# Optimization experiments

Hardware: AMD Instinct MI355X
Metric: run time of the kernel (lower is better)

The kernel has to match this reference:

```python
import jax, jax.numpy as jnp
import numpy as np

N, C, H, W = 8, 80, 200, 200
PRE_NMS_THRESH = 0.05
PRE_NMS_TOP_N = 1000
NMS_THRESH = 0.6
FPN_POST_NMS_TOP_N = 100
MIN_SIZE = 0.0
TO_REMOVE = 1.0
CLASS_OFFSET = 100000.0  # > any coordinate; separates classes for class-aware NMS


def setup_inputs() -> dict:
    key = jax.random.key(0)
    k1, k2, k3, k4, k5 = jax.random.split(key, 5)
    # logits shifted so sigmoid probs sit near the 0.05 threshold (realistic sparsity)
    box_cls = jax.random.normal(k1, (N, C, H, W), jnp.float32) - 3.0
    box_regression = jax.random.uniform(k2, (N, 4, H, W), jnp.float32) * 64.0
    centerness = jax.random.normal(k3, (N, 1, H, W), jnp.float32)
    locations = jax.random.uniform(k4, (H * W, 2), jnp.float32) * 1600.0
    image_sizes = jax.random.randint(k5, (N, 2), 800, 1600, jnp.int32)  # (h, w)
    return {"locations": locations, "box_cls": box_cls,
            "box_regression": box_regression, "centerness": centerness,
            "image_sizes": image_sizes}


def _pairwise_iou(boxes):
    x1, y1, x2, y2 = boxes[:, 0], boxes[:, 1], boxes[:, 2], boxes[:, 3]
    area = (x2 - x1 + TO_REMOVE) * (y2 - y1 + TO_REMOVE)  # [K]
    iw = jnp.clip(jnp.minimum(x2[:, None], x2[None, :]) - jnp.maximum(x1[:, None], x1[None, :]) + TO_REMOVE, 0.0)
    ih = jnp.clip(jnp.minimum(y2[:, None], y2[None, :]) - jnp.maximum(y1[:, None], y1[None, :]) + TO_REMOVE, 0.0)
    inter = iw * ih
    return inter / (area[:, None] + area[None, :] - inter)


def reference(locations, box_cls, box_regression, centerness, image_sizes):
    n, c, h, w = box_cls.shape
    # [N,C,H,W] -> [N,HW,C] probs; [N,4,H,W] -> [N,HW,4]; centerness -> [N,HW]
    cls_prob = jax.nn.sigmoid(box_cls.transpose(0, 2, 3, 1).reshape(n, -1, c))
    reg = box_regression.transpose(0, 2, 3, 1).reshape(n, -1, 4)
    cent = jax.nn.sigmoid(centerness.transpose(0, 2, 3, 1).reshape(n, -1))

    def per_image(p, r, ct, hw):
        # candidate mask on raw class probs (before centerness weighting), as in source
        cand = p > PRE_NMS_THRESH                      # [HW, C]
        scores = p * ct[:, None]                       # [HW, C]
        flat = jnp.where(cand, scores, -jnp.inf).reshape(-1)
        top_s, top_i = jax.lax.top_k(flat, PRE_NMS_TOP_N)   # sorted desc
        loc_idx = top_i // c
        labels = top_i % c + 1
        valid = top_s > 0.0
        l2 = locations[loc_idx]                        # [K, 2]
        rr = r[loc_idx]                                # [K, 4]
        boxes = jnp.concatenate([l2 - rr[:, :2], l2 + rr[:, 2:]], axis=-1)
        ih = hw[0].astype(jnp.float32)
        iw = hw[1].astype(jnp.float32)
        boxes = jnp.stack([jnp.clip(boxes[:, 0], 0.0, iw - 1.0),
                           jnp.clip(boxes[:, 1], 0.0, ih - 1.0),
                           jnp.clip(boxes[:, 2], 0.0, iw - 1.0),
                           jnp.clip(boxes[:, 3], 0.0, ih - 1.0)], axis=-1)
        bw = boxes[:, 2] - boxes[:, 0] + TO_REMOVE
        bh = boxes[:, 3] - boxes[:, 1] + TO_REMOVE
        valid = valid & (bw >= MIN_SIZE) & (bh >= MIN_SIZE)
        # class-aware NMS via per-class coordinate offset
        ob = boxes + labels.astype(jnp.float32)[:, None] * CLASS_OFFSET
        iou = _pairwise_iou(ob)                        # [K, K]
        K = PRE_NMS_TOP_N
        idxs = jnp.arange(K)
        def body(supp, i):
            keep_i = valid[i] & jnp.logical_not(supp[i])
            supp = supp | (keep_i & (iou[i] > NMS_THRESH) & (idxs != i))
            return supp, keep_i
        _, keep = jax.lax.scan(body, jnp.zeros(K, dtype=bool), idxs)
        fscores = jnp.where(keep & valid, top_s, -jnp.inf)
        fs, fi = jax.lax.top_k(fscores, FPN_POST_NMS_TOP_N)
        fv = fs > 0.0
        fb = boxes[fi] * fv[:, None].astype(boxes.dtype)
        fl = jnp.where(fv, labels[fi], 0).astype(jnp.float32)
        out_s = jnp.where(fv, jnp.sqrt(jnp.where(fv, fs, 1.0)), 0.0)  # sqrt of cls*centerness
        # [K_post, 6] = x1,y1,x2,y2,score,label
        return jnp.concatenate([fb, out_s[:, None], fl[:, None]], axis=-1)

    return jax.vmap(per_image)(cls_prob, reg, cent, image_sizes)
```

## Files before the change

### kernel.cpp

```cpp
#include <hip/hip_runtime.h>
#include <math.h>

#define NIMG 8
#define NCLS 80
#define HW 40000
#define M (NCLS*HW)
#define UBINS 4096
#define CANDL 4096
#define SPILL_CAP 65536
#define BCAP 1024
#define TOPK 1000
#define OUTK 100
#define PRE_T 0.05f
#define NMS_T 0.6f
#define FLOOR_S 0.25f
#define FLOOR_BITS 0x3E800000u
#define FLOOR_SAFE 0.2494f

__device__ unsigned int       g_scnt[NIMG][32];
__device__ unsigned int       g_ovf[NIMG];
__device__ float              g_xthr[NIMG * HW];
__device__ float              g_sct[NIMG * HW];
__device__ unsigned long long g_key[NIMG][SPILL_CAP];

__device__ __forceinline__ float sigmoid_exact(float x){
    return 1.0f / (1.0f + expf(-x));
}

__global__ void k0_init(const float* __restrict__ cent){
    int t = blockIdx.x * blockDim.x + threadIdx.x;
    if (t < NIMG * 32) ((unsigned int*)g_scnt)[t] = 0u;
    if (t < NIMG) g_ovf[t] = 0u;
    if (t < NIMG * HW){
        float pct = sigmoid_exact(cent[t]);
        g_sct[t] = pct;
        float a = FLOOR_SAFE / pct;
        float xt;
        if (a >= 1.0f) xt = 3.0e38f;
        else {
            float am = fminf(a, 0.98f);
            xt = logf(am / (1.0f - am));
        }
        g_xthr[t] = xt;
    }
}

__global__ void __launch_bounds__(1024) k1_spill(const float* __restrict__ cls){
    const int n   = blockIdx.y;
    const int tid = threadIdx.x;
    const int e0  = blockIdx.x * 4096 + tid * 4;
    __shared__ unsigned long long skey[BCAP];
    __shared__ unsigned int lcnt, lbase;
    if (tid == 0) lcnt = 0u;
    __syncthreads();
    if (e0 < M){
        const int c  = e0 / HW;
        const int hw = e0 - c * HW;
        float4 x  = *(const float4*)(cls + (size_t)n * M + e0);
        float4 th = *(const float4*)(g_xthr + n * HW + hw);
        #define SPILL1(J, XV) \
        if (XV >= (J==0?th.x:J==1?th.y:J==2?th.z:th.w)){ \
            float p_ = sigmoid_exact(XV); \
            if (p_ > PRE_T){ \
                float s_ = p_ * g_sct[n * HW + hw + J]; \
                unsigned long long key_ = ((unsigned long long)__float_as_uint(s_) << 32) \
                    | (unsigned long long)(0xFFFFFFFFu - (unsigned int)((hw + J) * NCLS + c)); \
                unsigned int pp_ = atomicAdd(&lcnt, 1u); \
                if (pp_ < BCAP) skey[pp_] = key_; \
            } \
        }
        SPILL1(0, x.x)
        SPILL1(1, x.y)
        SPILL1(2, x.z)
        SPILL1(3, x.w)
        #undef SPILL1
    }
    __syncthreads();
    unsigned int raw = lcnt;
    unsigned int cnt = raw < BCAP ? raw : BCAP;
    if (tid == 0){
        lbase = cnt ? atomicAdd(&g_scnt[n][0], cnt) : 0u;
        if (raw > BCAP) g_ovf[n] = 1u;
    }
    __syncthreads();
    unsigned int base = lbase;
    for (unsigned int i = tid; i < cnt; i += 1024){
        unsigned int pos = base + i;
        if (pos < SPILL_CAP) g_key[n][pos] = skey[i];
    }
}

struct SelPhase {
    unsigned int hist[UBINS];
    unsigned int cs[256];
    unsigned long long keysL[CANDL];
};
struct NmsPhase {
    float ox1[TOPK], oy1[TOPK], ox2[TOPK], oy2[TOPK], oar[TOPK];
    float bxs[TOPK][4];
    float sc[TOPK];
    int   lab[TOPK];
    unsigned char validf[TOPK];
    unsigned char supp[TOPK];
    int   keeplist[OUTK];
};
union KU { SelPhase sel; NmsPhase nms; };

__global__ void __launch_bounds__(1024) k2_select_nms(const float* __restrict__ cls,
                                                      const float* __restrict__ loc,
                                                      const float* __restrict__ reg,
                                                      const int*   __restrict__ imsz,
                                                      float* __restrict__ out){
    const int n = blockIdx.x;
    const int tid = threadIdx.x;
    const int lane = tid & 63;
    __shared__ KU u;
    __shared__ unsigned long long stop[TOPK];
    __shared__ unsigned int lcnt, c025, s_cut, s_flag;

    for (int i = tid; i < UBINS; i += 1024) u.sel.hist[i] = 0u;
    if (tid == 0){ lcnt = 0u; c025 = 0u; }
    if (tid < TOPK) stop[tid] = 0ull;
    __syncthreads();

    unsigned int scnt_raw = g_scnt[n][0];
    unsigned int S = scnt_raw < SPILL_CAP ? scnt_raw : SPILL_CAP;

    for (unsigned int i = tid; i < S; i += 1024){
        unsigned long long k = g_key[n][i];
        unsigned int bits = (unsigned int)(k >> 32);
        float s = __uint_as_float(bits);
        int bin = (int)(s * 4096.0f);
        atomicAdd(&u.sel.hist[bin], 1u);
        unsigned long long mb = __ballot(bits >= FLOOR_BITS);
        if (lane == 0 && mb) atomicAdd(&c025, (unsigned int)__popcll(mb));
    }
    __syncthreads();
    if (tid < 256){
        unsigned int s = 0;
        int base = tid * 16;
        #pragma unroll
        for (int i = 0; i < 16; ++i) s += u.sel.hist[base + i];
        u.sel.cs[tid] = s;
    }
    __syncthreads();
    if (tid == 0){
        unsigned int acc = 0; int cut = 0;
        int c = 255;
        for (; c >= 0; --c){ if (acc + u.sel.cs[c] >= TOPK) break; acc += u.sel.cs[c]; }
        unsigned int Cest = 0;
        if (c >= 0){
            int b = c*16 + 15;
            for (;; --b){
                if (acc + u.sel.hist[b] >= TOPK || b == c*16){ cut = b; break; }
                acc += u.sel.hist[b];
            }
            Cest = acc + u.sel.hist[cut];
        }
        unsigned int fl = (scnt_raw > SPILL_CAP) || g_ovf[n] || (c < 0) ||
                          (c025 < TOPK) || (Cest > CANDL) ? 1u : 0u;
        s_cut = (unsigned int)cut; s_flag = fl;
    }
    __syncthreads();

    if (s_flag){
        for (int i = tid; i < UBINS; i += 1024) u.sel.hist[i] = 0u;
        __syncthreads();
        const float* cls_n = cls + (size_t)n * M;
        const float* sct_n = g_sct + n * HW;
        for (int e = tid; e < M; e += 1024){
            float p = sigmoid_exact(cls_n[e]);
            if (p > PRE_T){
                int c = e / HW; int hw = e - c * HW;
                float s = p * sct_n[hw];
                atomicAdd(&u.sel.hist[(int)(s * 4096.0f)], 1u);
            }
        }
        __syncthreads();
        if (tid < 256){
            unsigned int s = 0;
            int base = tid * 16;
            #pragma unroll
            for (int i = 0; i < 16; ++i) s += u.sel.hist[base + i];
            u.sel.cs[tid] = s;
        }
        __syncthreads();
        if (tid == 0){
            unsigned int acc = 0; int cut = 0; int c = 255;
            for (; c >= 0; --c){ if (acc + u.sel.cs[c] >= TOPK) break; acc += u.sel.cs[c]; }
            if (c >= 0){
                int b = c*16 + 15;
                for (;; --b){ acc += u.sel.hist[b]; if (acc >= TOPK || b == c*16) break; }
                cut = b;
            }
            while (acc > CANDL && cut < UBINS){ acc -= u.sel.hist[cut]; cut++; }
            s_cut = (unsigned int)cut;
        }
        __syncthreads();
        unsigned int cutb = s_cut;
        for (int e = tid; e < M; e += 1024){
            float p = sigmoid_exact(cls_n[e]);
            if (p > PRE_T){
                int c = e / HW; int hw = e - c * HW;
                float s = p * sct_n[hw];
                if ((int)(s * 4096.0f) >= (int)cutb){
                    unsigned int pos = atomicAdd(&lcnt, 1u);
                    if (pos < CANDL){
                        unsigned int idx = (unsigned int)(hw * NCLS + c);
                        u.sel.keysL[pos] = ((unsigned long long)__float_as_uint(s) << 32)
                                         | (unsigned long long)(0xFFFFFFFFu - idx);
                    }
                }
            }
        }
    } else {
        unsigned int cutb = s_cut;
        for (unsigned int i = tid; i < S; i += 1024){
            unsigned long long k = g_key[n][i];
            float s = __uint_as_float((unsigned int)(k >> 32));
            bool pass = ((unsigned int)(int)(s * 4096.0f)) >= cutb;
            unsigned long long mb = __ballot(pass);
            unsigned int wcnt = (unsigned int)__popcll(mb);
            unsigned int base = 0;
            if (lane == 0 && wcnt) base = atomicAdd(&lcnt, wcnt);
            base = (unsigned int)__builtin_amdgcn_readfirstlane((int)base);
            if (pass){
                unsigned int p = base + (unsigned int)__popcll(mb & ((1ull << lane) - 1ull));
                if (p < CANDL) u.sel.keysL[p] = k;
            }
        }
    }
    __syncthreads();

    int C = (int)(lcnt < CANDL ? lcnt : CANDL);
    for (int i = tid; i < C; i += 1024){
        unsigned long long k = u.sel.keysL[i];
        int rank = 0;
        for (int j = 0; j < C; ++j) rank += (u.sel.keysL[j] > k) ? 1 : 0;
        if (rank < TOPK) stop[rank] = k;
    }
    __syncthreads();

    float rx1 = 0.f, ry1 = 0.f, rx2 = -1.f, ry2 = -1.f, rar = 1.f;
    float ihh = (float)imsz[2*n + 0];
    float iww = (float)imsz[2*n + 1];
    unsigned long long kk = (tid < TOPK) ? stop[tid] : 0ull;
    __syncthreads();
    if (tid < TOPK){
        unsigned int bits = (unsigned int)(kk >> 32);
        float s = __uint_as_float(bits);
        u.nms.supp[tid] = 0;
        if (s > 0.0f){
            unsigned int idx = 0xFFFFFFFFu - (unsigned int)(kk & 0xFFFFFFFFull);
            int hw = (int)(idx / NCLS);
            int c  = (int)(idx % NCLS);
            int l  = c + 1;
            float x  = loc[2*hw], y = loc[2*hw + 1];
            float r0 = reg[((size_t)n*4 + 0)*HW + hw];
            float r1 = reg[((size_t)n*4 + 1)*HW + hw];
            float r2 = reg[((size_t)n*4 + 2)*HW + hw];
            float r3 = reg[((size_t)n*4 + 3)*HW + hw];
            float x1 = fminf(fmaxf(x - r0, 0.0f), iww - 1.0f);
            float y1 = fminf(fmaxf(y - r1, 0.0f), ihh - 1.0f);
            float x2 = fminf(fmaxf(x + r2, 0.0f), iww - 1.0f);
            float y2 = fminf(fmaxf(y + r3, 0.0f), ihh - 1.0f);
            u.nms.bxs[tid][0] = x1; u.nms.bxs[tid][1] = y1;
            u.nms.bxs[tid][2] = x2; u.nms.bxs[tid][3] = y2;
            float off = (float)l * 100000.0f;
            float a1 = x1 + off, b1 = y1 + off, a2 = x2 + off, b2 = y2 + off;
            float ar = (a2 - a1 + 1.0f) * (b2 - b1 + 1.0f);
            u.nms.ox1[tid] = a1; u.nms.oy1[tid] = b1;
            u.nms.ox2[tid] = a2; u.nms.oy2[tid] = b2; u.nms.oar[tid] = ar;
            rx1 = a1; ry1 = b1; rx2 = a2; ry2 = b2; rar = ar;
            u.nms.sc[tid] = s; u.nms.lab[tid] = l; u.nms.validf[tid] = 1;
        } else {
            u.nms.validf[tid] = 0; u.nms.sc[tid] = 0.0f; u.nms.lab[tid] = 0;
            u.nms.bxs[tid][0] = u.nms.bxs[tid][1] = 0.0f;
            u.nms.bxs[tid][2] = u.nms.bxs[tid][3] = 0.0f;
            u.nms.ox1[tid] = 0.f; u.nms.oy1[tid] = 0.f;
            u.nms.ox2[tid] = -1.f; u.nms.oy2[tid] = -1.f; u.nms.oar[tid] = 1.f;
        }
    }
    __syncthreads();

    int cnt = 0;
    for (int i = 0; i < TOPK; ++i){
        bool keep_i = u.nms.validf[i] && !u.nms.supp[i];
        if (keep_i){
            if (tid == 0) u.nms.keeplist[cnt] = i;
            if (tid < TOPK && tid != i){
                float ix1 = fmaxf(u.nms.ox1[i], rx1);
                float iy1 = fmaxf(u.nms.oy1[i], ry1);
                float ix2 = fminf(u.nms.ox2[i], rx2);
                float iy2 = fminf(u.nms.oy2[i], ry2);
                float iw_ = fmaxf(ix2 - ix1 + 1.0f, 0.0f);
                float ih_ = fmaxf(iy2 - iy1 + 1.0f, 0.0f);
                float inter = iw_ * ih_;
                float iou = inter / (u.nms.oar[i] + rar - inter);
                if (iou > NMS_T) u.nms.supp[tid] = 1;
            }
            cnt++;
            __syncthreads();
            if (cnt == OUTK) break;
        }
    }
    __syncthreads();

    if (tid < OUTK){
        float r0=0.f,r1=0.f,r2=0.f,r3=0.f,r4=0.f,r5=0.f;
        if (tid < cnt){
            int i = u.nms.keeplist[tid];
            r0 = u.nms.bxs[i][0]; r1 = u.nms.bxs[i][1];
            r2 = u.nms.bxs[i][2]; r3 = u.nms.bxs[i][3];
            r4 = sqrtf(u.nms.sc[i]); r5 = (float)u.nms.lab[i];
        }
        float* o = out + ((size_t)n*OUTK + tid)*6;
        o[0]=r0; o[1]=r1; o[2]=r2; o[3]=r3; o[4]=r4; o[5]=r5;
    }
}

extern "C" void kernel_launch(void* const* d_in, const int* in_sizes, int n_in,
                              void* d_out, int out_size, void* d_ws, size_t ws_size,
                              hipStream_t stream){
    const float* loc  = (const float*)d_in[0];
    const float* cls  = (const float*)d_in[1];
    const float* reg  = (const float*)d_in[2];
    const float* cent = (const float*)d_in[3];
    const int*   imsz = (const int*)d_in[4];
    float* out = (float*)d_out;

    hipLaunchKernelGGL(k0_init,       dim3(625),                 dim3(512),  0, stream, cent);
    hipLaunchKernelGGL(k1_spill,      dim3((M+4095)/4096, NIMG), dim3(1024), 0, stream, cls);
    hipLaunchKernelGGL(k2_select_nms, dim3(NIMG),                dim3(1024), 0, stream,
                       cls, loc, reg, imsz, out);
}
```

Measured before the change: 291.5 us.

## Replace rank sort with bitonic sort and parallelize NMS per class in waves

```diff
diff --git a/kernel.cpp b/kernel.cpp
--- a/kernel.cpp
+++ b/kernel.cpp
@@ -100,9 +100,14 @@
     float bxs[TOPK][4];
     float sc[TOPK];
     int   lab[TOPK];
+    int   keeplist[OUTK];
+    unsigned int  Wc[16][80];
+    unsigned int  coff[81];
+    unsigned int  wcnt[16];
+    unsigned short ord[1024];
     unsigned char validf[TOPK];
     unsigned char supp[TOPK];
-    int   keeplist[OUTK];
+    unsigned char keepf[1024];
 };
 union KU { SelPhase sel; NmsPhase nms; };
 
@@ -114,12 +119,13 @@
     const int n = blockIdx.x;
     const int tid = threadIdx.x;
     const int lane = tid & 63;
+    const int wv   = tid >> 6;
     __shared__ KU u;
     __shared__ unsigned long long stop[TOPK];
-    __shared__ unsigned int lcnt, c025, s_cut, s_flag;
+    __shared__ unsigned int lcnt, c025, s_cut, s_flag, s_nmsfb, s_cnt;
 
     for (int i = tid; i < UBINS; i += 1024) u.sel.hist[i] = 0u;
-    if (tid == 0){ lcnt = 0u; c025 = 0u; }
+    if (tid == 0){ lcnt = 0u; c025 = 0u; s_nmsfb = 0u; }
     if (tid < TOPK) stop[tid] = 0ull;
     __syncthreads();
 
@@ -220,9 +226,9 @@
             float s = __uint_as_float((unsigned int)(k >> 32));
             bool pass = ((unsigned int)(int)(s * 4096.0f)) >= cutb;
             unsigned long long mb = __ballot(pass);
-            unsigned int wcnt = (unsigned int)__popcll(mb);
+            unsigned int wcnt_ = (unsigned int)__popcll(mb);
             unsigned int base = 0;
-            if (lane == 0 && wcnt) base = atomicAdd(&lcnt, wcnt);
+            if (lane == 0 && wcnt_) base = atomicAdd(&lcnt, wcnt_);
             base = (unsigned int)__builtin_amdgcn_readfirstlane((int)base);
             if (pass){
                 unsigned int p = base + (unsigned int)__popcll(mb & ((1ull << lane) - 1ull));
@@ -233,11 +239,31 @@
     __syncthreads();
 
     int C = (int)(lcnt < CANDL ? lcnt : CANDL);
-    for (int i = tid; i < C; i += 1024){
-        unsigned long long k = u.sel.keysL[i];
-        int rank = 0;
-        for (int j = 0; j < C; ++j) rank += (u.sel.keysL[j] > k) ? 1 : 0;
-        if (rank < TOPK) stop[rank] = k;
+    if (C <= 2048){
+        int Nsort = (C <= 1024) ? 1024 : 2048;
+        for (int i = C + tid; i < Nsort; i += 1024) u.sel.keysL[i] = 0ull;
+        __syncthreads();
+        for (int k = 2; k <= Nsort; k <<= 1){
+            for (int j = k >> 1; j > 0; j >>= 1){
+                if (tid < (Nsort >> 1)){
+                    int i  = ((tid & ~(j - 1)) << 1) | (tid & (j - 1));
+                    int p2 = i | j;
+                    unsigned long long a = u.sel.keysL[i];
+                    unsigned long long b = u.sel.keysL[p2];
+                    bool up = ((i & k) == 0);
+                    if (up ? (a < b) : (a > b)){ u.sel.keysL[i] = b; u.sel.keysL[p2] = a; }
+                }
+                __syncthreads();
+            }
+        }
+        if (tid < TOPK) stop[tid] = u.sel.keysL[tid];
+    } else {
+        for (int i = tid; i < C; i += 1024){
+            unsigned long long k = u.sel.keysL[i];
+            int rank = 0;
+            for (int j = 0; j < C; ++j) rank += (u.sel.keysL[j] > k) ? 1 : 0;
+            if (rank < TOPK) stop[rank] = k;
+        }
     }
     __syncthreads();
 
@@ -246,6 +272,11 @@
     float iww = (float)imsz[2*n + 1];
     unsigned long long kk = (tid < TOPK) ? stop[tid] : 0ull;
     __syncthreads();
+
+    u.nms.keepf[tid] = 0;
+    { unsigned int* wz = &u.nms.Wc[0][0];
+      for (int i = tid; i < 16*80; i += 1024) wz[i] = 0u; }
+
     if (tid < TOPK){
         unsigned int bits = (unsigned int)(kk >> 32);
         float s = __uint_as_float(bits);
@@ -283,29 +314,115 @@
     }
     __syncthreads();
 
-    int cnt = 0;
-    for (int i = 0; i < TOPK; ++i){
-        bool keep_i = u.nms.validf[i] && !u.nms.supp[i];
-        if (keep_i){
-            if (tid == 0) u.nms.keeplist[cnt] = i;
-            if (tid < TOPK && tid != i){
-                float ix1 = fmaxf(u.nms.ox1[i], rx1);
-                float iy1 = fmaxf(u.nms.oy1[i], ry1);
-                float ix2 = fminf(u.nms.ox2[i], rx2);
-                float iy2 = fminf(u.nms.oy2[i], ry2);
-                float iw_ = fmaxf(ix2 - ix1 + 1.0f, 0.0f);
-                float ih_ = fmaxf(iy2 - iy1 + 1.0f, 0.0f);
-                float inter = iw_ * ih_;
-                float iou = inter / (u.nms.oar[i] + rar - inter);
-                if (iou > NMS_T) u.nms.supp[tid] = 1;
-            }
-            cnt++;
-            __syncthreads();
-            if (cnt == OUTK) break;
-        }
-    }
-    __syncthreads();
-
+    int mk = -1;
+    if (tid < TOPK && u.nms.validf[tid]) mk = u.nms.lab[tid] - 1;
+    if (mk >= 0) atomicAdd(&u.nms.Wc[wv][mk], 1u);
+    __syncthreads();
+    if (tid < NCLS){
+        unsigned int acc = 0;
+        for (int w = 0; w < 16; ++w){
+            unsigned int v = u.nms.Wc[w][tid];
+            u.nms.Wc[w][tid] = acc;
+            acc += v;
+        }
+        u.nms.coff[tid] = acc;
+        if (acc > 64) atomicOr(&s_nmsfb, 1u);
+    }
+    __syncthreads();
+    if (tid == 0){
+        unsigned int acc = 0;
+        for (int k = 0; k < NCLS; ++k){ unsigned int t = u.nms.coff[k]; u.nms.coff[k] = acc; acc += t; }
+        u.nms.coff[NCLS] = acc;
+    }
+    __syncthreads();
+
+    if (!s_nmsfb){
+        int below = 0;
+        for (int l = 0; l < 64; ++l){
+            int ok = __shfl(mk, l);
+            below += (l < lane && ok == mk) ? 1 : 0;
+        }
+        if (mk >= 0){
+            unsigned int pos = u.nms.coff[mk] + u.nms.Wc[wv][mk] + (unsigned int)below;
+            u.nms.ord[pos] = (unsigned short)tid;
+        }
+        __syncthreads();
+
+        for (int k = wv; k < NCLS; k += 16){
+            int base = (int)u.nms.coff[k];
+            int ck   = (int)u.nms.coff[k + 1] - base;
+            if (ck <= 0) continue;
+            int rr = (lane < ck) ? (int)u.nms.ord[base + lane] : -1;
+            float bx1 = 0.f, by1 = 0.f, bx2 = -1.f, by2 = -1.f, bar = 1.f;
+            if (rr >= 0){
+                bx1 = u.nms.ox1[rr]; by1 = u.nms.oy1[rr];
+                bx2 = u.nms.ox2[rr]; by2 = u.nms.oy2[rr]; bar = u.nms.oar[rr];
+            }
+            int sup = 0;
+            for (int p = 0; p < ck; ++p){
+                int keep_p = !__shfl(sup, p);
+                if (keep_p){
+                    float px1 = __shfl(bx1, p), py1 = __shfl(by1, p);
+                    float px2 = __shfl(bx2, p), py2 = __shfl(by2, p);
+                    float par = __shfl(bar, p);
+                    if (lane > p && rr >= 0){
+                        float ix1 = fmaxf(px1, bx1);
+                        float iy1 = fmaxf(py1, by1);
+                        float ix2 = fminf(px2, bx2);
+                        float iy2 = fminf(py2, by2);
+                        float iw_ = fmaxf(ix2 - ix1 + 1.0f, 0.0f);
+                        float ih_ = fmaxf(iy2 - iy1 + 1.0f, 0.0f);
+                        float inter = iw_ * ih_;
+                        float iou = inter / (par + bar - inter);
+                        if (iou > NMS_T) sup = 1;
+                    }
+                }
+            }
+            if (rr >= 0) u.nms.keepf[rr] = sup ? 0 : 1;
+        }
+        __syncthreads();
+
+        int kf = (int)u.nms.keepf[tid];
+        unsigned long long mb = __ballot(kf != 0);
+        if (lane == 0) u.nms.wcnt[wv] = (unsigned int)__popcll(mb);
+        __syncthreads();
+        if (tid == 0){
+            unsigned int acc = 0;
+            for (int w = 0; w < 16; ++w){ unsigned int t = u.nms.wcnt[w]; u.nms.wcnt[w] = acc; acc += t; }
+            s_cnt = acc < OUTK ? acc : OUTK;
+        }
+        __syncthreads();
+        if (kf){
+            unsigned int slot = u.nms.wcnt[wv] + (unsigned int)__popcll(mb & ((1ull << lane) - 1ull));
+            if (slot < OUTK) u.nms.keeplist[slot] = tid;
+        }
+    } else {
+        int cnt = 0;
+        for (int i = 0; i < TOPK; ++i){
+            bool keep_i = u.nms.validf[i] && !u.nms.supp[i];
+            if (keep_i){
+                if (tid == 0) u.nms.keeplist[cnt] = i;
+                if (tid < TOPK && tid != i){
+                    float ix1 = fmaxf(u.nms.ox1[i], rx1);
+                    float iy1 = fmaxf(u.nms.oy1[i], ry1);
+                    float ix2 = fminf(u.nms.ox2[i], rx2);
+                    float iy2 = fminf(u.nms.oy2[i], ry2);
+                    float iw_ = fmaxf(ix2 - ix1 + 1.0f, 0.0f);
+                    float ih_ = fmaxf(iy2 - iy1 + 1.0f, 0.0f);
+                    float inter = iw_ * ih_;
+                    float iou = inter / (u.nms.oar[i] + rar - inter);
+                    if (iou > NMS_T) u.nms.supp[tid] = 1;
+                }
+                cnt++;
+                __syncthreads();
+                if (cnt == OUTK) break;
+            }
+        }
+        if (tid == 0) s_cnt = (unsigned int)(cnt < OUTK ? cnt : OUTK);
+    }
+    __syncthreads();
+
+    int cnt = (int)s_cnt;
     if (tid < OUTK){
         float r0=0.f,r1=0.f,r2=0.f,r3=0.f,r4=0.f,r5=0.f;
         if (tid < cnt){
```

After: 257.4 us. -11.7%, faster.
